# Kernel tuning notes

Hardware: AMD Instinct MI355X
Metric: run time of the kernel (lower is better)

The kernel has to match this reference:

```python
import jax, jax.numpy as jnp
import numpy as np

B, S, D = 1, 2048, 1024
NH, NKV, HD = 16, 4, 64
N_REP = NH // NKV


def _rope_tables(seq_len, half_dim, base=10000.0):
    inv_freq = 1.0 / (base ** (np.arange(0, half_dim, dtype=np.float32) / half_dim))
    t = np.arange(seq_len, dtype=np.float32)
    freqs = np.outer(t, inv_freq)  # (S, HD//2)
    return jnp.asarray(np.cos(freqs)), jnp.asarray(np.sin(freqs))


def setup_inputs() -> dict:
    key = jax.random.key(0)
    ks = jax.random.split(key, 5)
    x = jax.random.normal(ks[0], (B, S, D), dtype=jnp.float32)
    rope_cos, rope_sin = _rope_tables(S, HD // 2)
    sd = 1.0 / np.sqrt(D)
    Wq = jax.random.normal(ks[1], (D, NH * HD), dtype=jnp.float32) * sd
    Wk = jax.random.normal(ks[2], (D, NKV * HD), dtype=jnp.float32) * sd
    Wv = jax.random.normal(ks[3], (D, NKV * HD), dtype=jnp.float32) * sd
    Wo = jax.random.normal(ks[4], (NH * HD, D), dtype=jnp.float32) * sd
    return {"x": x, "rope_cos": rope_cos, "rope_sin": rope_sin,
            "Wq": Wq, "Wk": Wk, "Wv": Wv, "Wo": Wo}


def _apply_rope(t, cos, sin):
    # t: (B, H, S, HD); cos/sin: (S, HD//2). Rotate-half convention.
    t1, t2 = jnp.split(t, 2, axis=-1)
    c = cos[None, None, :, :]
    s = sin[None, None, :, :]
    return jnp.concatenate([t1 * c - t2 * s, t2 * c + t1 * s], axis=-1)


def reference(x, rope_cos, rope_sin, Wq, Wk, Wv, Wo):
    b, s, _ = x.shape
    # projections -> (B, H, S, HD)
    q = (x @ Wq).reshape(b, s, NH, HD).transpose(0, 2, 1, 3)
    k = (x @ Wk).reshape(b, s, NKV, HD).transpose(0, 2, 1, 3)
    v = (x @ Wv).reshape(b, s, NKV, HD).transpose(0, 2, 1, 3)
    q = _apply_rope(q, rope_cos, rope_sin)
    k = _apply_rope(k, rope_cos, rope_sin)
    # GQA expansion (repeat_interleave on head axis)
    k = jnp.repeat(k, N_REP, axis=1)
    v = jnp.repeat(v, N_REP, axis=1)
    scale = HD ** -0.5
    scores = jnp.einsum('bhqd,bhkd->bhqk', q, k) * scale
    causal = jnp.tril(jnp.ones((s, s), dtype=bool))
    scores = jnp.where(causal[None, None], scores, jnp.float32(-jnp.inf))
    attn = jax.nn.softmax(scores, axis=-1)
    out = jnp.einsum('bhqk,bhkd->bhqd', attn, v)  # (B, H, S, HD)
    out = out.transpose(0, 2, 1, 3).reshape(b, s, NH * HD)
    return out @ Wo
```

## Files before the change

kernel.cpp:

```cpp
#include <hip/hip_runtime.h>

typedef unsigned short ushort_t;
typedef __attribute__((ext_vector_type(8))) short short8;
typedef __attribute__((ext_vector_type(4))) float f32x4;
typedef __attribute__((ext_vector_type(4))) unsigned short ushort4v;
typedef __attribute__((ext_vector_type(8))) unsigned short ushort8v;

#define S_LEN 2048
#define D_MODEL 1024
#define NH 16
#define NKV 4
#define HD 64

__device__ __forceinline__ ushort_t f2bf(float f) {
    unsigned u = __float_as_uint(f);
    u += 0x7fffu + ((u >> 16) & 1u);
    return (ushort_t)(u >> 16);
}

__device__ __forceinline__ void cp16(void* lds, const void* g) {
    __builtin_amdgcn_global_load_lds(
        (__attribute__((address_space(1))) void*)g,
        (__attribute__((address_space(3))) void*)lds, 16, 0, 0);
}

__global__ __launch_bounds__(256) void convert_x_kernel(
    const float* __restrict__ x, ushort_t* __restrict__ xb)
{
    const int i = (blockIdx.x * 256 + threadIdx.x) * 4;
    float4 v = *(const float4*)(x + i);
    ushort4v o = { f2bf(v.x), f2bf(v.y), f2bf(v.z), f2bf(v.w) };
    *(ushort4v*)(xb + i) = o;
}

__global__ __launch_bounds__(256) void wtrans_kernel(
    const float* __restrict__ Wq, const float* __restrict__ Wk,
    const float* __restrict__ Wv, const float* __restrict__ Wo,
    ushort_t* __restrict__ WqT, ushort_t* __restrict__ WkT,
    ushort_t* __restrict__ WvT, ushort_t* __restrict__ WoT)
{
    __shared__ ushort_t T[64 * 72];
    const float* W; ushort_t* WT; int N;
    switch (blockIdx.z) {
        case 0:  W = Wq; WT = WqT; N = 1024; break;
        case 1:  W = Wk; WT = WkT; N = 256;  break;
        case 2:  W = Wv; WT = WvT; N = 256;  break;
        default: W = Wo; WT = WoT; N = 1024; break;
    }
    const int n0 = blockIdx.y * 64;
    if (n0 >= N) return;
    const int k0 = blockIdx.x * 64;
    const int t  = threadIdx.x;
    const int kr = t >> 4, nc = (t & 15) * 4;
    #pragma unroll
    for (int p = 0; p < 4; ++p) {
        const int k = kr + p * 16;
        float4 v = *(const float4*)(W + (size_t)(k0 + k) * N + n0 + nc);
        T[(nc + 0) * 72 + k] = f2bf(v.x);
        T[(nc + 1) * 72 + k] = f2bf(v.y);
        T[(nc + 2) * 72 + k] = f2bf(v.z);
        T[(nc + 3) * 72 + k] = f2bf(v.w);
    }
    __syncthreads();
    const int n = t >> 2, seg = (t & 3) * 16;
    ushort8v a = *(ushort8v*)&T[n * 72 + seg];
    ushort8v b = *(ushort8v*)&T[n * 72 + seg + 8];
    *(ushort8v*)(WT + (size_t)(n0 + n) * 1024 + k0 + seg)     = a;
    *(ushort8v*)(WT + (size_t)(n0 + n) * 1024 + k0 + seg + 8) = b;
}

__global__ __launch_bounds__(256, 2) void gemm_qkv_mfma(
    const ushort_t* __restrict__ xb, const ushort_t* __restrict__ WqT,
    const ushort_t* __restrict__ WkT, const ushort_t* __restrict__ WvT,
    const float* __restrict__ rc, const float* __restrict__ rs,
    ushort_t* __restrict__ Qb, ushort_t* __restrict__ Kb,
    ushort_t* __restrict__ Vtb)
{
    __shared__ ushort_t As[2][64 * 64];
    __shared__ ushort_t Bs[2][128 * 64];

    const int t = threadIdx.x;
    const int lane = t & 63, wave = t >> 6;
    const int wr = wave >> 1, wc = wave & 1;
    const int quad = lane >> 4, l15 = lane & 15;
    const int lq = lane >> 3, lr = lane & 7;
    const int swz_st = (lr ^ lq) * 8;
    const int l7 = l15 & 7;
    const int fsw0 = (quad ^ l7) * 8;
    const int fsw1 = ((quad + 4) ^ l7) * 8;

    const int m0 = blockIdx.x * 64;
    const int cy = blockIdx.y;

    const ushort_t* WT; int nloc;
    if (cy < 8)       { WT = WqT; nloc = cy * 128; }
    else if (cy < 10) { WT = WkT; nloc = (cy - 8) * 128; }
    else              { WT = WvT; nloc = (cy - 10) * 128; }

    f32x4 acc[2][4];
    #pragma unroll
    for (int i = 0; i < 2; ++i)
        #pragma unroll
        for (int j = 0; j < 4; ++j) acc[i][j] = (f32x4)0.f;

    auto stage = [&](int buf, int k0) {
        #pragma unroll
        for (int i = 0; i < 2; ++i) {
            const int r = wave * 16 + i * 8 + lq;
            cp16(&As[buf][(wave * 16 + i * 8) * 64],
                 xb + (size_t)(m0 + r) * 1024 + k0 + swz_st);
        }
        #pragma unroll
        for (int i = 0; i < 4; ++i) {
            const int r = wave * 32 + i * 8 + lq;
            cp16(&Bs[buf][(wave * 32 + i * 8) * 64],
                 WT + (size_t)(nloc + r) * 1024 + k0 + swz_st);
        }
    };

    stage(0, 0);
    __syncthreads();

    for (int kk = 0; kk < 16; ++kk) {
        const int cur = kk & 1;
        if (kk + 1 < 16) stage(cur ^ 1, (kk + 1) * 64);

        const ushort_t* Ac = &As[cur][0];
        const ushort_t* Bc = &Bs[cur][0];
        #pragma unroll
        for (int h = 0; h < 2; ++h) {
            const int fsw = h ? fsw1 : fsw0;
            short8 av[2], bv[4];
            #pragma unroll
            for (int i = 0; i < 2; ++i)
                av[i] = *(const short8*)&Ac[(wr * 32 + i * 16 + l15) * 64 + fsw];
            #pragma unroll
            for (int j = 0; j < 4; ++j)
                bv[j] = *(const short8*)&Bc[(wc * 64 + j * 16 + l15) * 64 + fsw];
            #pragma unroll
            for (int i = 0; i < 2; ++i)
                #pragma unroll
                for (int j = 0; j < 4; ++j)
                    acc[i][j] = __builtin_amdgcn_mfma_f32_16x16x32_bf16(
                        av[i], bv[j], acc[i][j], 0, 0, 0);
        }
        __syncthreads();
    }

    if (cy < 10) {
        ushort_t* dst = (cy < 8) ? Qb : Kb;
        const int h = ((cy < 8) ? cy : (cy - 8)) * 2 + wc;
        #pragma unroll
        for (int i = 0; i < 2; ++i) {
            #pragma unroll
            for (int j = 0; j < 2; ++j) {
                const int d = j * 16 + l15;
                #pragma unroll
                for (int reg = 0; reg < 4; ++reg) {
                    const int s = m0 + wr * 32 + i * 16 + quad * 4 + reg;
                    const float c  = rc[s * 32 + d];
                    const float sn = rs[s * 32 + d];
                    const float v1 = acc[i][j][reg];
                    const float v2 = acc[i][j + 2][reg];
                    dst[((size_t)h * S_LEN + s) * HD + d]      = f2bf(v1 * c - v2 * sn);
                    dst[((size_t)h * S_LEN + s) * HD + d + 32] = f2bf(v2 * c + v1 * sn);
                }
            }
        }
    } else {
        const int vh = (cy - 10) * 2 + wc;
        #pragma unroll
        for (int i = 0; i < 2; ++i) {
            const int s0 = m0 + wr * 32 + i * 16 + quad * 4;
            #pragma unroll
            for (int j = 0; j < 4; ++j) {
                const int d = j * 16 + l15;
                ushort4v o = { f2bf(acc[i][j][0]), f2bf(acc[i][j][1]),
                               f2bf(acc[i][j][2]), f2bf(acc[i][j][3]) };
                *(ushort4v*)&Vtb[((size_t)vh * HD + d) * S_LEN + s0] = o;
            }
        }
    }
}

__global__ __launch_bounds__(256, 2) void attn_mfma(
    const ushort_t* __restrict__ Qb, const ushort_t* __restrict__ Kb,
    const ushort_t* __restrict__ Vtb, ushort_t* __restrict__ attnb)
{
    __shared__ ushort_t Ks[2][64 * 64];
    __shared__ ushort_t Vs[2][64 * 64];
    __shared__ ushort_t Ps[4][16 * 72];

    const int t = threadIdx.x;
    const int lane = t & 63, wave = t >> 6;
    const int quad = lane >> 4, l15 = lane & 15;
    const int lq = lane >> 3, lr = lane & 7;
    const int swz_st = (lr ^ lq) * 8;
    const int l7 = l15 & 7;
    const int fsw0 = (quad ^ l7) * 8;
    const int fsw1 = ((quad + 4) ^ l7) * 8;

    const int h  = blockIdx.x;
    const int y  = blockIdx.y;
    const int qt = (y < 16) ? y : 47 - y;
    const int q0 = qt * 64;
    const int kvh = h >> 2;
    const int qrow0 = q0 + wave * 16;

    const ushort_t* Qg = Qb + ((size_t)h * S_LEN + qrow0) * HD;
    const ushort_t* Kg = Kb + (size_t)kvh * S_LEN * HD;
    const ushort_t* Vg = Vtb + (size_t)kvh * HD * S_LEN;

    short8 aq0 = *(const short8*)(Qg + (size_t)l15 * HD + quad * 8);
    short8 aq1 = *(const short8*)(Qg + (size_t)l15 * HD + 32 + quad * 8);

    float ps4[4] = {0.f, 0.f, 0.f, 0.f};
    f32x4 Oacc[4];
    #pragma unroll
    for (int jb = 0; jb < 4; ++jb) Oacc[jb] = (f32x4)0.f;

    const int ntiles = qt + 1;

    auto stage = [&](int buf, int kvo) {
        #pragma unroll
        for (int i = 0; i < 2; ++i) {
            const int r = wave * 16 + i * 8 + lq;
            cp16(&Ks[buf][(wave * 16 + i * 8) * 64],
                 Kg + (size_t)(kvo + r) * 64 + swz_st);
            cp16(&Vs[buf][(wave * 16 + i * 8) * 64],
                 Vg + (size_t)r * 2048 + kvo + swz_st);
        }
    };

    stage(0, 0);
    __syncthreads();

    ushort_t* Pw = &Ps[wave][0];

    for (int tile = 0; tile < ntiles; ++tile) {
        const int cur = tile & 1;
        if (tile + 1 < ntiles) stage(cur ^ 1, (tile + 1) * 64);

        const ushort_t* Kc = &Ks[cur][0];
        const ushort_t* Vc = &Vs[cur][0];

        f32x4 sv[4];
        #pragma unroll
        for (int jb = 0; jb < 4; ++jb) {
            short8 b0 = *(const short8*)&Kc[(jb * 16 + l15) * 64 + fsw0];
            short8 b1 = *(const short8*)&Kc[(jb * 16 + l15) * 64 + fsw1];
            f32x4 z = (f32x4)0.f;
            z = __builtin_amdgcn_mfma_f32_16x16x32_bf16(aq0, b0, z, 0, 0, 0);
            z = __builtin_amdgcn_mfma_f32_16x16x32_bf16(aq1, b1, z, 0, 0, 0);
            sv[jb] = z;
        }

        const bool diag = (tile == ntiles - 1);
        const int kv0 = tile * 64;
        #pragma unroll
        for (int jb = 0; jb < 4; ++jb) {
            const int col = kv0 + jb * 16 + l15;
            #pragma unroll
            for (int reg = 0; reg < 4; ++reg) {
                float e = __expf(sv[jb][reg] * 0.125f);
                if (diag && col > qrow0 + quad * 4 + reg) e = 0.f;
                sv[jb][reg] = e;
                ps4[reg] += e;
            }
        }

        #pragma unroll
        for (int jb = 0; jb < 4; ++jb)
            #pragma unroll
            for (int reg = 0; reg < 4; ++reg)
                Pw[(quad * 4 + reg) * 72 + jb * 16 + l15] = f2bf(sv[jb][reg]);
        short8 p0 = *(const short8*)&Pw[l15 * 72 + quad * 8];
        short8 p1 = *(const short8*)&Pw[l15 * 72 + 32 + quad * 8];

        #pragma unroll
        for (int jb = 0; jb < 4; ++jb) {
            short8 v0 = *(const short8*)&Vc[(jb * 16 + l15) * 64 + fsw0];
            short8 v1 = *(const short8*)&Vc[(jb * 16 + l15) * 64 + fsw1];
            Oacc[jb] = __builtin_amdgcn_mfma_f32_16x16x32_bf16(p0, v0, Oacc[jb], 0, 0, 0);
            Oacc[jb] = __builtin_amdgcn_mfma_f32_16x16x32_bf16(p1, v1, Oacc[jb], 0, 0, 0);
        }

        __syncthreads();
    }

    #pragma unroll
    for (int reg = 0; reg < 4; ++reg) {
        float l = ps4[reg];
        l += __shfl_xor(l, 1);
        l += __shfl_xor(l, 2);
        l += __shfl_xor(l, 4);
        l += __shfl_xor(l, 8);
        const float inv = 1.f / l;
        const int s = qrow0 + quad * 4 + reg;
        #pragma unroll
        for (int jb = 0; jb < 4; ++jb)
            attnb[(size_t)s * D_MODEL + h * HD + jb * 16 + l15] =
                f2bf(Oacc[jb][reg] * inv);
    }
}

__global__ __launch_bounds__(256, 2) void gemm_out_mfma(
    const ushort_t* __restrict__ Ab, const ushort_t* __restrict__ WoT,
    float* __restrict__ out)
{
    __shared__ ushort_t As[2][64 * 64];
    __shared__ ushort_t Bs[2][128 * 64];

    const int t = threadIdx.x;
    const int lane = t & 63, wave = t >> 6;
    const int wr = wave >> 1, wc = wave & 1;
    const int quad = lane >> 4, l15 = lane & 15;
    const int lq = lane >> 3, lr = lane & 7;
    const int swz_st = (lr ^ lq) * 8;
    const int l7 = l15 & 7;
    const int fsw0 = (quad ^ l7) * 8;
    const int fsw1 = ((quad + 4) ^ l7) * 8;

    const int m0 = blockIdx.x * 64;
    const int n0 = blockIdx.y * 128;

    f32x4 acc[2][4];
    #pragma unroll
    for (int i = 0; i < 2; ++i)
        #pragma unroll
        for (int j = 0; j < 4; ++j) acc[i][j] = (f32x4)0.f;

    auto stage = [&](int buf, int k0) {
        #pragma unroll
        for (int i = 0; i < 2; ++i) {
            const int r = wave * 16 + i * 8 + lq;
            cp16(&As[buf][(wave * 16 + i * 8) * 64],
                 Ab + (size_t)(m0 + r) * 1024 + k0 + swz_st);
        }
        #pragma unroll
        for (int i = 0; i < 4; ++i) {
            const int r = wave * 32 + i * 8 + lq;
            cp16(&Bs[buf][(wave * 32 + i * 8) * 64],
                 WoT + (size_t)(n0 + r) * 1024 + k0 + swz_st);
        }
    };

    stage(0, 0);
    __syncthreads();

    for (int kk = 0; kk < 16; ++kk) {
        const int cur = kk & 1;
        if (kk + 1 < 16) stage(cur ^ 1, (kk + 1) * 64);

        const ushort_t* Ac = &As[cur][0];
        const ushort_t* Bc = &Bs[cur][0];
        #pragma unroll
        for (int h = 0; h < 2; ++h) {
            const int fsw = h ? fsw1 : fsw0;
            short8 av[2], bv[4];
            #pragma unroll
            for (int i = 0; i < 2; ++i)
                av[i] = *(const short8*)&Ac[(wr * 32 + i * 16 + l15) * 64 + fsw];
            #pragma unroll
            for (int j = 0; j < 4; ++j)
                bv[j] = *(const short8*)&Bc[(wc * 64 + j * 16 + l15) * 64 + fsw];
            #pragma unroll
            for (int i = 0; i < 2; ++i)
                #pragma unroll
                for (int j = 0; j < 4; ++j)
                    acc[i][j] = __builtin_amdgcn_mfma_f32_16x16x32_bf16(
                        av[i], bv[j], acc[i][j], 0, 0, 0);
        }
        __syncthreads();
    }

    #pragma unroll
    for (int i = 0; i < 2; ++i)
        #pragma unroll
        for (int reg = 0; reg < 4; ++reg) {
            const int s = m0 + wr * 32 + i * 16 + quad * 4 + reg;
            #pragma unroll
            for (int j = 0; j < 4; ++j)
                out[(size_t)s * D_MODEL + n0 + wc * 64 + j * 16 + l15] = acc[i][j][reg];
        }
}

extern "C" void kernel_launch(void* const* d_in, const int* in_sizes, int n_in,
                              void* d_out, int out_size, void* d_ws, size_t ws_size,
                              hipStream_t stream)
{
    const float* x  = (const float*)d_in[0];
    const float* rc = (const float*)d_in[1];
    const float* rs = (const float*)d_in[2];
    const float* Wq = (const float*)d_in[3];
    const float* Wk = (const float*)d_in[4];
    const float* Wv = (const float*)d_in[5];
    const float* Wo = (const float*)d_in[6];
    float* out = (float*)d_out;

    ushort_t* xb   = (ushort_t*)d_ws;
    ushort_t* WqT  = xb   + (size_t)2048 * 1024;
    ushort_t* WkT  = WqT  + (size_t)1024 * 1024;
    ushort_t* WvT  = WkT  + (size_t)256 * 1024;
    ushort_t* WoT  = WvT  + (size_t)256 * 1024;
    ushort_t* Qb   = WoT  + (size_t)1024 * 1024;
    ushort_t* Kb   = Qb   + (size_t)NH * S_LEN * HD;
    ushort_t* Vtb  = Kb   + (size_t)NKV * S_LEN * HD;
    ushort_t* attnb= Vtb  + (size_t)NKV * HD * S_LEN;

    convert_x_kernel<<<2048, 256, 0, stream>>>(x, xb);
    wtrans_kernel<<<dim3(16, 16, 4), 256, 0, stream>>>(Wq, Wk, Wv, Wo,
                                                       WqT, WkT, WvT, WoT);
    gemm_qkv_mfma<<<dim3(32, 12), 256, 0, stream>>>(xb, WqT, WkT, WvT,
                                                    rc, rs, Qb, Kb, Vtb);
    attn_mfma<<<dim3(NH, 32), 256, 0, stream>>>(Qb, Kb, Vtb, attnb);
    gemm_out_mfma<<<dim3(32, 8), 256, 0, stream>>>(attnb, WoT, out);
}
```

Measured before the change: 149.0 us.

## Merge prep kernels, stage two KV tiles per round, shrink output GEMM tile

Folds the x-to-bf16 conversion into the weight-transpose kernel as an extra z-slice, removing one launch. The attention kernel now stages two 64-wide K/V tiles per double-buffer round, halving the number of barriers per block at the cost of twice the LDS footprint, which may reduce occupancy. The output GEMM tile drops from 64x128 to 64x64, doubling the grid to 512 blocks for better CU fill but lowering per-block data reuse.

```diff
diff --git a/kernel.cpp b/kernel.cpp
--- a/kernel.cpp
+++ b/kernel.cpp
@@ -24,21 +24,26 @@
         (__attribute__((address_space(3))) void*)lds, 16, 0, 0);
 }
 
-__global__ __launch_bounds__(256) void convert_x_kernel(
-    const float* __restrict__ x, ushort_t* __restrict__ xb)
-{
-    const int i = (blockIdx.x * 256 + threadIdx.x) * 4;
-    float4 v = *(const float4*)(x + i);
-    ushort4v o = { f2bf(v.x), f2bf(v.y), f2bf(v.z), f2bf(v.w) };
-    *(ushort4v*)(xb + i) = o;
-}
-
-__global__ __launch_bounds__(256) void wtrans_kernel(
+__global__ __launch_bounds__(256) void prep_kernel(
+    const float* __restrict__ x, ushort_t* __restrict__ xb,
     const float* __restrict__ Wq, const float* __restrict__ Wk,
     const float* __restrict__ Wv, const float* __restrict__ Wo,
     ushort_t* __restrict__ WqT, ushort_t* __restrict__ WkT,
     ushort_t* __restrict__ WvT, ushort_t* __restrict__ WoT)
 {
+    const int t = threadIdx.x;
+    if (blockIdx.z == 4) {
+        const int b  = blockIdx.y * 16 + blockIdx.x;
+        const int i0 = (b * 256 + t) * 4;
+        #pragma unroll
+        for (int rep = 0; rep < 8; ++rep) {
+            const int i = i0 + rep * 262144;
+            float4 v = *(const float4*)(x + i);
+            ushort4v o = { f2bf(v.x), f2bf(v.y), f2bf(v.z), f2bf(v.w) };
+            *(ushort4v*)(xb + i) = o;
+        }
+        return;
+    }
     __shared__ ushort_t T[64 * 72];
     const float* W; ushort_t* WT; int N;
     switch (blockIdx.z) {
@@ -50,7 +55,6 @@
     const int n0 = blockIdx.y * 64;
     if (n0 >= N) return;
     const int k0 = blockIdx.x * 64;
-    const int t  = threadIdx.x;
     const int kr = t >> 4, nc = (t & 15) * 4;
     #pragma unroll
     for (int p = 0; p < 4; ++p) {
@@ -187,8 +191,8 @@
     const ushort_t* __restrict__ Qb, const ushort_t* __restrict__ Kb,
     const ushort_t* __restrict__ Vtb, ushort_t* __restrict__ attnb)
 {
-    __shared__ ushort_t Ks[2][64 * 64];
-    __shared__ ushort_t Vs[2][64 * 64];
+    __shared__ ushort_t Ks[2][2][64 * 64];
+    __shared__ ushort_t Vs[2][2][64 * 64];
     __shared__ ushort_t Ps[4][16 * 72];
 
     const int t = threadIdx.x;
@@ -219,17 +223,19 @@
     #pragma unroll
     for (int jb = 0; jb < 4; ++jb) Oacc[jb] = (f32x4)0.f;
 
-    const int ntiles = qt + 1;
-
-    auto stage = [&](int buf, int kvo) {
-        #pragma unroll
-        for (int i = 0; i < 2; ++i) {
-            const int r = wave * 16 + i * 8 + lq;
-            cp16(&Ks[buf][(wave * 16 + i * 8) * 64],
-                 Kg + (size_t)(kvo + r) * 64 + swz_st);
-            cp16(&Vs[buf][(wave * 16 + i * 8) * 64],
-                 Vg + (size_t)r * 2048 + kvo + swz_st);
-        }
+    const int nround = (qt + 2) >> 1;
+
+    auto stage = [&](int buf, int kvbase) {
+        #pragma unroll
+        for (int u = 0; u < 2; ++u)
+            #pragma unroll
+            for (int i = 0; i < 2; ++i) {
+                const int r = wave * 16 + i * 8 + lq;
+                cp16(&Ks[buf][u][(wave * 16 + i * 8) * 64],
+                     Kg + (size_t)(kvbase + u * 64 + r) * 64 + swz_st);
+                cp16(&Vs[buf][u][(wave * 16 + i * 8) * 64],
+                     Vg + (size_t)r * 2048 + kvbase + u * 64 + swz_st);
+            }
     };
 
     stage(0, 0);
@@ -237,52 +243,56 @@
 
     ushort_t* Pw = &Ps[wave][0];
 
-    for (int tile = 0; tile < ntiles; ++tile) {
-        const int cur = tile & 1;
-        if (tile + 1 < ntiles) stage(cur ^ 1, (tile + 1) * 64);
-
-        const ushort_t* Kc = &Ks[cur][0];
-        const ushort_t* Vc = &Vs[cur][0];
-
-        f32x4 sv[4];
-        #pragma unroll
-        for (int jb = 0; jb < 4; ++jb) {
-            short8 b0 = *(const short8*)&Kc[(jb * 16 + l15) * 64 + fsw0];
-            short8 b1 = *(const short8*)&Kc[(jb * 16 + l15) * 64 + fsw1];
-            f32x4 z = (f32x4)0.f;
-            z = __builtin_amdgcn_mfma_f32_16x16x32_bf16(aq0, b0, z, 0, 0, 0);
-            z = __builtin_amdgcn_mfma_f32_16x16x32_bf16(aq1, b1, z, 0, 0, 0);
-            sv[jb] = z;
-        }
-
-        const bool diag = (tile == ntiles - 1);
-        const int kv0 = tile * 64;
-        #pragma unroll
-        for (int jb = 0; jb < 4; ++jb) {
-            const int col = kv0 + jb * 16 + l15;
-            #pragma unroll
-            for (int reg = 0; reg < 4; ++reg) {
-                float e = __expf(sv[jb][reg] * 0.125f);
-                if (diag && col > qrow0 + quad * 4 + reg) e = 0.f;
-                sv[jb][reg] = e;
-                ps4[reg] += e;
-            }
-        }
-
-        #pragma unroll
-        for (int jb = 0; jb < 4; ++jb)
-            #pragma unroll
-            for (int reg = 0; reg < 4; ++reg)
-                Pw[(quad * 4 + reg) * 72 + jb * 16 + l15] = f2bf(sv[jb][reg]);
-        short8 p0 = *(const short8*)&Pw[l15 * 72 + quad * 8];
-        short8 p1 = *(const short8*)&Pw[l15 * 72 + 32 + quad * 8];
-
-        #pragma unroll
-        for (int jb = 0; jb < 4; ++jb) {
-            short8 v0 = *(const short8*)&Vc[(jb * 16 + l15) * 64 + fsw0];
-            short8 v1 = *(const short8*)&Vc[(jb * 16 + l15) * 64 + fsw1];
-            Oacc[jb] = __builtin_amdgcn_mfma_f32_16x16x32_bf16(p0, v0, Oacc[jb], 0, 0, 0);
-            Oacc[jb] = __builtin_amdgcn_mfma_f32_16x16x32_bf16(p1, v1, Oacc[jb], 0, 0, 0);
+    for (int round = 0; round < nround; ++round) {
+        const int cur = round & 1;
+        if (round + 1 < nround) stage(cur ^ 1, (round + 1) * 128);
+
+        #pragma unroll
+        for (int u = 0; u < 2; ++u) {
+            const int kv0 = round * 128 + u * 64;
+            if (kv0 > q0 + 63) break;
+            const ushort_t* Kc = &Ks[cur][u][0];
+            const ushort_t* Vc = &Vs[cur][u][0];
+
+            f32x4 sv[4];
+            #pragma unroll
+            for (int jb = 0; jb < 4; ++jb) {
+                short8 b0 = *(const short8*)&Kc[(jb * 16 + l15) * 64 + fsw0];
+                short8 b1 = *(const short8*)&Kc[(jb * 16 + l15) * 64 + fsw1];
+                f32x4 z = (f32x4)0.f;
+                z = __builtin_amdgcn_mfma_f32_16x16x32_bf16(aq0, b0, z, 0, 0, 0);
+                z = __builtin_amdgcn_mfma_f32_16x16x32_bf16(aq1, b1, z, 0, 0, 0);
+                sv[jb] = z;
+            }
+
+            const bool diag = (kv0 == q0);
+            #pragma unroll
+            for (int jb = 0; jb < 4; ++jb) {
+                const int col = kv0 + jb * 16 + l15;
+                #pragma unroll
+                for (int reg = 0; reg < 4; ++reg) {
+                    float e = __expf(sv[jb][reg] * 0.125f);
+                    if (diag && col > qrow0 + quad * 4 + reg) e = 0.f;
+                    sv[jb][reg] = e;
+                    ps4[reg] += e;
+                }
+            }
+
+            #pragma unroll
+            for (int jb = 0; jb < 4; ++jb)
+                #pragma unroll
+                for (int reg = 0; reg < 4; ++reg)
+                    Pw[(quad * 4 + reg) * 72 + jb * 16 + l15] = f2bf(sv[jb][reg]);
+            short8 p0 = *(const short8*)&Pw[l15 * 72 + quad * 8];
+            short8 p1 = *(const short8*)&Pw[l15 * 72 + 32 + quad * 8];
+
+            #pragma unroll
+            for (int jb = 0; jb < 4; ++jb) {
+                short8 v0 = *(const short8*)&Vc[(jb * 16 + l15) * 64 + fsw0];
+                short8 v1 = *(const short8*)&Vc[(jb * 16 + l15) * 64 + fsw1];
+                Oacc[jb] = __builtin_amdgcn_mfma_f32_16x16x32_bf16(p0, v0, Oacc[jb], 0, 0, 0);
+                Oacc[jb] = __builtin_amdgcn_mfma_f32_16x16x32_bf16(p1, v1, Oacc[jb], 0, 0, 0);
+            }
         }
 
         __syncthreads();
@@ -309,7 +319,7 @@
     float* __restrict__ out)
 {
     __shared__ ushort_t As[2][64 * 64];
-    __shared__ ushort_t Bs[2][128 * 64];
+    __shared__ ushort_t Bs[2][64 * 64];
 
     const int t = threadIdx.x;
     const int lane = t & 63, wave = t >> 6;
@@ -322,13 +332,13 @@
     const int fsw1 = ((quad + 4) ^ l7) * 8;
 
     const int m0 = blockIdx.x * 64;
-    const int n0 = blockIdx.y * 128;
-
-    f32x4 acc[2][4];
+    const int n0 = blockIdx.y * 64;
+
+    f32x4 acc[2][2];
     #pragma unroll
     for (int i = 0; i < 2; ++i)
         #pragma unroll
-        for (int j = 0; j < 4; ++j) acc[i][j] = (f32x4)0.f;
+        for (int j = 0; j < 2; ++j) acc[i][j] = (f32x4)0.f;
 
     auto stage = [&](int buf, int k0) {
         #pragma unroll
@@ -336,11 +346,7 @@
             const int r = wave * 16 + i * 8 + lq;
             cp16(&As[buf][(wave * 16 + i * 8) * 64],
                  Ab + (size_t)(m0 + r) * 1024 + k0 + swz_st);
-        }
-        #pragma unroll
-        for (int i = 0; i < 4; ++i) {
-            const int r = wave * 32 + i * 8 + lq;
-            cp16(&Bs[buf][(wave * 32 + i * 8) * 64],
+            cp16(&Bs[buf][(wave * 16 + i * 8) * 64],
                  WoT + (size_t)(n0 + r) * 1024 + k0 + swz_st);
         }
     };
@@ -357,17 +363,17 @@
         #pragma unroll
         for (int h = 0; h < 2; ++h) {
             const int fsw = h ? fsw1 : fsw0;
-            short8 av[2], bv[4];
+            short8 av[2], bv[2];
             #pragma unroll
             for (int i = 0; i < 2; ++i)
                 av[i] = *(const short8*)&Ac[(wr * 32 + i * 16 + l15) * 64 + fsw];
             #pragma unroll
-            for (int j = 0; j < 4; ++j)
-                bv[j] = *(const short8*)&Bc[(wc * 64 + j * 16 + l15) * 64 + fsw];
+            for (int j = 0; j < 2; ++j)
+                bv[j] = *(const short8*)&Bc[(wc * 32 + j * 16 + l15) * 64 + fsw];
             #pragma unroll
             for (int i = 0; i < 2; ++i)
                 #pragma unroll
-                for (int j = 0; j < 4; ++j)
+                for (int j = 0; j < 2; ++j)
                     acc[i][j] = __builtin_amdgcn_mfma_f32_16x16x32_bf16(
                         av[i], bv[j], acc[i][j], 0, 0, 0);
         }
@@ -380,8 +386,8 @@
         for (int reg = 0; reg < 4; ++reg) {
             const int s = m0 + wr * 32 + i * 16 + quad * 4 + reg;
             #pragma unroll
-            for (int j = 0; j < 4; ++j)
-                out[(size_t)s * D_MODEL + n0 + wc * 64 + j * 16 + l15] = acc[i][j][reg];
+            for (int j = 0; j < 2; ++j)
+                out[(size_t)s * D_MODEL + n0 + wc * 32 + j * 16 + l15] = acc[i][j][reg];
         }
 }
 
@@ -408,11 +414,10 @@
     ushort_t* Vtb  = Kb   + (size_t)NKV * S_LEN * HD;
     ushort_t* attnb= Vtb  + (size_t)NKV * HD * S_LEN;
 
-    convert_x_kernel<<<2048, 256, 0, stream>>>(x, xb);
-    wtrans_kernel<<<dim3(16, 16, 4), 256, 0, stream>>>(Wq, Wk, Wv, Wo,
-                                                       WqT, WkT, WvT, WoT);
+    prep_kernel<<<dim3(16, 16, 5), 256, 0, stream>>>(x, xb, Wq, Wk, Wv, Wo,
+                                                     WqT, WkT, WvT, WoT);
     gemm_qkv_mfma<<<dim3(32, 12), 256, 0, stream>>>(xb, WqT, WkT, WvT,
                                                     rc, rs, Qb, Kb, Vtb);
     attn_mfma<<<dim3(NH, 32), 256, 0, stream>>>(Qb, Kb, Vtb, attnb);
-    gemm_out_mfma<<<dim3(32, 8), 256, 0, stream>>>(attnb, WoT, out);
-}
+    gemm_out_mfma<<<dim3(32, 16), 256, 0, stream>>>(attnb, WoT, out);
+}
```

New measurement: 145.0 us. 1.03x faster.
